# Kernel tuning notes

Measured on AMD Instinct MI355X. Metric: run time of the kernel, lower is better.

Reference implementation:

```python
import jax, jax.numpy as jnp
import numpy as np

N_NODES = 100000
N_EDGES = 3200000
N_FEAT = 128
N_GRAPHS = 64


def setup_inputs() -> dict:
    key = jax.random.key(0)
    ks = jax.random.split(key, 8)
    x = jax.random.normal(ks[0], (N_NODES, N_FEAT), dtype=jnp.float32)
    edge_index = jax.random.randint(ks[1], (2, N_EDGES), 0, N_NODES, dtype=jnp.int64)
    batch = jnp.sort(jax.random.randint(ks[2], (N_NODES,), 0, N_GRAPHS, dtype=jnp.int64))
    # GCNConv weights (glorot-style scale) and biases
    W1 = jax.random.normal(ks[3], (N_FEAT, 32), dtype=jnp.float32) / np.sqrt(N_FEAT)
    b1 = jnp.zeros((32,), dtype=jnp.float32)
    W2 = jax.random.normal(ks[4], (32, 16), dtype=jnp.float32) / np.sqrt(32.0)
    b2 = jnp.zeros((16,), dtype=jnp.float32)
    lin_w = jax.random.normal(ks[5], (16, 1), dtype=jnp.float32) / np.sqrt(16.0)
    lin_b = jnp.zeros((1,), dtype=jnp.float32)
    return {"x": x, "edge_index": edge_index, "batch": batch,
            "W1": W1, "b1": b1, "W2": W2, "b2": b2,
            "lin_w": lin_w, "lin_b": lin_b}


def _gcn_conv(x, W, b, src, dst, deg_inv_sqrt, n_nodes):
    # transform first (fewer features downstream when out_dim < in_dim)
    xw = x @ W  # [N, out]
    norm = deg_inv_sqrt[src] * deg_inv_sqrt[dst]  # [E+N]
    msg = xw[src] * norm[:, None]  # gather + scale
    out = jax.ops.segment_sum(msg, dst, num_segments=n_nodes)  # scatter-add
    return out + b


def reference(x, edge_index, batch, W1, b1, W2, b2, lin_w, lin_b):
    n_nodes = x.shape[0]
    self_loop = jnp.arange(n_nodes, dtype=edge_index.dtype)
    src = jnp.concatenate([edge_index[0], self_loop])
    dst = jnp.concatenate([edge_index[1], self_loop])
    # symmetric GCN normalization with self-loops
    deg = jax.ops.segment_sum(jnp.ones_like(src, dtype=x.dtype), dst,
                              num_segments=n_nodes)
    deg_inv_sqrt = jnp.where(deg > 0, jax.lax.rsqrt(jnp.maximum(deg, 1.0)), 0.0)

    h = _gcn_conv(x, W1, b1, src, dst, deg_inv_sqrt, n_nodes)
    h = jax.nn.relu(h)
    # F.dropout with training=False (eval) is identity
    h = _gcn_conv(h, W2, b2, src, dst, deg_inv_sqrt, n_nodes)

    # global_mean_pool over batch index
    sums = jax.ops.segment_sum(h, batch, num_segments=N_GRAPHS)  # [G,16]
    cnts = jax.ops.segment_sum(jnp.ones((n_nodes,), dtype=h.dtype), batch,
                               num_segments=N_GRAPHS)
    pooled = sums / jnp.maximum(cnts, 1.0)[:, None]
    return pooled @ lin_w + lin_b  # [G,1]
```

## Files before the change

kernel.cpp:

```cpp
#include <hip/hip_runtime.h>

#define NN 100000
#define NE 3200000
#define NF 128
#define C1 32
#define C2 16
#define NG 64
#define BKT_SH 7
#define BKT_W  128
#define NBKT   782
#define CH     8192
#define NW     391
#define RSTR   784
#define MAPCAP 6400

#define OFF_BCNT  0
#define OFF_POOL  1024
#define OFF_CNTF  2048
#define OFF_RUN   2304
#define OFF_ROW   308848
#define OFF_DIS   408864
#define OFF_EDG   508864
#define OFF_XS1   OFF_EDG
#define OFF_XS2B  (OFF_EDG + NE)
#define OFF_COL   (OFF_XS2B + NN*8)

__device__ __forceinline__ unsigned pack_bf2(float a, float b) {
    unsigned ua = __float_as_uint(a);
    unsigned ub = __float_as_uint(b);
    ua = (ua + 0x7fffu + ((ua >> 16) & 1u)) >> 16;
    ub = (ub + 0x7fffu + ((ub >> 16) & 1u)) & 0xffff0000u;
    return ua | ub;
}
__device__ __forceinline__ float2 unpack_bf2(unsigned u) {
    return make_float2(__uint_as_float(u << 16), __uint_as_float(u & 0xffff0000u));
}
__device__ __forceinline__ void accum8(float* a, uint4 q) {
    float2 f0 = unpack_bf2(q.x), f1 = unpack_bf2(q.y);
    float2 f2 = unpack_bf2(q.z), f3 = unpack_bf2(q.w);
    a[0] += f0.x; a[1] += f0.y; a[2] += f1.x; a[3] += f1.y;
    a[4] += f2.x; a[5] += f2.y; a[6] += f3.x; a[7] += f3.y;
}

__global__ __launch_bounds__(512) void k_part(
    const int* __restrict__ S, const int* __restrict__ D,
    unsigned* __restrict__ edgebuf, int* __restrict__ runstart,
    int* __restrict__ bcnt)
{
    __shared__ int lhist[1024];
    __shared__ int lstart[1024];
    __shared__ int lcur[NBKT];
    __shared__ int wsum[8];
    __shared__ unsigned lsort[CH];
    const int w = blockIdx.x;
    const int t = threadIdx.x;
    const int e0 = w * CH;
    const int n = min(CH, NE - e0);
    const int n4 = n >> 2;
    const int4* __restrict__ S4 = (const int4*)(S + e0);
    const int4* __restrict__ D4 = (const int4*)(D + e0);

    for (int i = t; i < 1024; i += 512) lhist[i] = 0;
    __syncthreads();
    for (int i = t; i < n4; i += 512) {
        int4 d = D4[i];
        atomicAdd(&lhist[(unsigned)d.x >> BKT_SH], 1);
        atomicAdd(&lhist[(unsigned)d.y >> BKT_SH], 1);
        atomicAdd(&lhist[(unsigned)d.z >> BKT_SH], 1);
        atomicAdd(&lhist[(unsigned)d.w >> BKT_SH], 1);
    }
    __syncthreads();
    for (int i = t; i < NBKT; i += 512) atomicAdd(&bcnt[i], lhist[i]);

    int c0 = lhist[t * 2 + 0], c1 = lhist[t * 2 + 1];
    int ts = c0 + c1;
    const int lane = t & 63, wv = t >> 6;
    int sc = ts;
    #pragma unroll
    for (int off = 1; off < 64; off <<= 1) {
        int v = __shfl_up(sc, off, 64);
        if (lane >= off) sc += v;
    }
    if (lane == 63) wsum[wv] = sc;
    __syncthreads();
    int wo = 0;
    #pragma unroll
    for (int i = 0; i < 8; ++i) wo += (i < wv) ? wsum[i] : 0;
    int excl = sc - ts + wo;
    lstart[t * 2 + 0] = excl;
    lstart[t * 2 + 1] = excl + c0;
    __syncthreads();

    for (int i = t; i < 783; i += 512) runstart[w * RSTR + i] = lstart[i];
    for (int i = t; i < NBKT; i += 512) lcur[i] = lstart[i];
    __syncthreads();
    for (int i = t; i < n4; i += 512) {
        int4 s = S4[i];
        int4 d = D4[i];
        { int p = atomicAdd(&lcur[(unsigned)d.x >> BKT_SH], 1);
          lsort[p] = ((unsigned)s.x << BKT_SH) | ((unsigned)d.x & (BKT_W - 1)); }
        { int p = atomicAdd(&lcur[(unsigned)d.y >> BKT_SH], 1);
          lsort[p] = ((unsigned)s.y << BKT_SH) | ((unsigned)d.y & (BKT_W - 1)); }
        { int p = atomicAdd(&lcur[(unsigned)d.z >> BKT_SH], 1);
          lsort[p] = ((unsigned)s.z << BKT_SH) | ((unsigned)d.z & (BKT_W - 1)); }
        { int p = atomicAdd(&lcur[(unsigned)d.w >> BKT_SH], 1);
          lsort[p] = ((unsigned)s.w << BKT_SH) | ((unsigned)d.w & (BKT_W - 1)); }
    }
    __syncthreads();
    {
        uint4* __restrict__ eb4 = (uint4*)(edgebuf + e0);
        const uint4* __restrict__ ls4 = (const uint4*)lsort;
        for (int i = t; i < n4; i += 512) eb4[i] = ls4[i];
    }
}

__global__ __launch_bounds__(256) void k_fillfused(
    const unsigned* __restrict__ edgebuf, const int* __restrict__ runstart,
    const int* __restrict__ bcnt,
    int* __restrict__ rowstart, float* __restrict__ dis, int* __restrict__ colidx)
{
    __shared__ int rl[NW];
    __shared__ int pfx[NW];
    __shared__ int basea[NW];
    __shared__ unsigned short map[MAPCAP];
    __shared__ int lcnt[BKT_W];
    __shared__ int lcur[BKT_W];
    __shared__ int wsum[4];
    __shared__ int hs1;
    const int b = blockIdx.x;
    const int t = threadIdx.x;
    const int lane = t & 63, wv = t >> 6;

    int accp = 0;
    for (int i = t; i < b; i += 256) accp += bcnt[i];
    #pragma unroll
    for (int off = 1; off < 64; off <<= 1) accp += __shfl_xor(accp, off, 64);
    if (lane == 0) wsum[wv] = accp;

    for (int w = t; w < NW; w += 256) {
        int s0 = runstart[w * RSTR + b];
        int s1 = runstart[w * RSTR + b + 1];
        basea[w] = s0;
        rl[w] = s1 - s0;
    }
    if (t < BKT_W) lcnt[t] = 0;
    __syncthreads();
    const int bs = wsum[0] + wsum[1] + wsum[2] + wsum[3];

    int w0 = t * 2;
    int c0 = (w0 < NW) ? rl[w0] : 0;
    int c1 = (w0 + 1 < NW) ? rl[w0 + 1] : 0;
    int ts = c0 + c1;
    int sc = ts;
    #pragma unroll
    for (int off = 1; off < 64; off <<= 1) {
        int v = __shfl_up(sc, off, 64);
        if (lane >= off) sc += v;
    }
    __syncthreads();
    if (lane == 63) wsum[wv] = sc;
    __syncthreads();
    int wo = 0;
    #pragma unroll
    for (int i = 0; i < 4; ++i) wo += (i < wv) ? wsum[i] : 0;
    const int total = wsum[0] + wsum[1] + wsum[2] + wsum[3];
    int excl0 = sc - ts + wo;
    if (w0 < NW)     pfx[w0]     = excl0;
    if (w0 + 1 < NW) pfx[w0 + 1] = excl0 + c0;
    __syncthreads();

    for (int w = t; w < NW; w += 256) {
        int p = pfx[w], len = rl[w];
        basea[w] = w * CH + basea[w] - p;
        for (int i = 0; i < len; ++i) map[p + i] = (unsigned short)w;
    }
    __syncthreads();
    for (int j = t; j < total; j += 256) {
        unsigned p = edgebuf[basea[map[j]] + j];
        atomicAdd(&lcnt[p & (BKT_W - 1)], 1);
    }
    __syncthreads();

    int myc = 0, sc2 = 0;
    if (t < BKT_W) {
        myc = lcnt[t];
        sc2 = myc;
        #pragma unroll
        for (int off = 1; off < 64; off <<= 1) {
            int v = __shfl_up(sc2, off, 64);
            if (lane >= off) sc2 += v;
        }
        if (t == 63) hs1 = sc2;
    }
    __syncthreads();
    if (t < BKT_W) {
        int excl = sc2 - myc + ((t >= 64) ? hs1 : 0);
        int node = b * BKT_W + t;
        if (node < NN) {
            rowstart[node] = bs + excl;
            dis[node] = rsqrtf((float)myc + 1.0f);
        }
        lcur[t] = bs + excl;
    }
    if (b == 0 && t == 0) rowstart[NN] = NE;
    __syncthreads();
    for (int j = t; j < total; j += 256) {
        unsigned p = edgebuf[basea[map[j]] + j];
        int pos = atomicAdd(&lcur[p & (BKT_W - 1)], 1);
        colidx[pos] = (int)(p >> BKT_SH);
    }
}

__global__ __launch_bounds__(256) void k_gemm1(
    const float* __restrict__ x, const float* __restrict__ W1,
    const float* __restrict__ dis,
    unsigned* __restrict__ xs1)
{
    __shared__ float xls[128 * 33];
    __shared__ float wls[32 * 32];
    const int t = threadIdx.x;
    const int tc = t & 7;
    const int tr = t >> 3;
    const int base = blockIdx.x * 128;

    float a[4][4] = {};

    for (int k0 = 0; k0 < NF; k0 += 32) {
        {
            int i = t * 4;
            int kk = i >> 5, c = i & 31;
            *(float4*)&wls[kk * 32 + c] = *(const float4*)&W1[(k0 + kk) * C1 + c];
        }
        #pragma unroll
        for (int r = 0; r < 4; ++r) {
            int n = (t >> 3) + r * 32;
            int j = (t & 7) * 4;
            int node = base + n;
            float4 v = make_float4(0.f, 0.f, 0.f, 0.f);
            if (node < NN) v = *(const float4*)&x[(long long)node * NF + k0 + j];
            xls[n * 33 + j + 0] = v.x;
            xls[n * 33 + j + 1] = v.y;
            xls[n * 33 + j + 2] = v.z;
            xls[n * 33 + j + 3] = v.w;
        }
        __syncthreads();
        #pragma unroll 8
        for (int kk = 0; kk < 32; ++kk) {
            float4 w = *(const float4*)&wls[kk * 32 + tc * 4];
            #pragma unroll
            for (int i = 0; i < 4; ++i) {
                float xv = xls[(tr * 4 + i) * 33 + kk];
                a[i][0] = fmaf(xv, w.x, a[i][0]);
                a[i][1] = fmaf(xv, w.y, a[i][1]);
                a[i][2] = fmaf(xv, w.z, a[i][2]);
                a[i][3] = fmaf(xv, w.w, a[i][3]);
            }
        }
        __syncthreads();
    }
    #pragma unroll
    for (int i = 0; i < 4; ++i) {
        int node = base + tr * 4 + i;
        if (node < NN) {
            float dv = dis[node];
            uint2 o;
            o.x = pack_bf2(a[i][0] * dv, a[i][1] * dv);
            o.y = pack_bf2(a[i][2] * dv, a[i][3] * dv);
            *(uint2*)&xs1[node * 16 + tc * 2] = o;
        }
    }
}

__global__ __launch_bounds__(256) void k_gather1(
    const unsigned* __restrict__ xs1, const int* __restrict__ colidx,
    const int* __restrict__ rowstart, const float* __restrict__ dis,
    const float* __restrict__ b1, const float* __restrict__ W2,
    unsigned* __restrict__ xs2b)
{
    __shared__ float w2s[C1 * C2];
    __shared__ float hrow[64 * 33];
    const int t = threadIdx.x;
    if (t < 128) *(float4*)&w2s[t * 4] = *(const float4*)&W2[t * 4];
    const int l = t & 3;
    const int n = t >> 2;
    const int v = blockIdx.x * 64 + n;
    const bool valid = v < NN;

    float a0[8] = {}, a1[8] = {};
    float dv = 0.f;
    if (valid) {
        const int start = rowstart[v];
        const int num = rowstart[v + 1] - start;
        const int* __restrict__ cp = &colidx[start];
        const uint4* __restrict__ tb = (const uint4*)xs1;
        accum8(a0, tb[v * 4 + l]);
        int i = 0;
        for (; i + 8 <= num; i += 8) {
            int s0 = cp[i],   s1 = cp[i+1], s2 = cp[i+2], s3 = cp[i+3];
            int s4 = cp[i+4], s5 = cp[i+5], s6 = cp[i+6], s7 = cp[i+7];
            uint4 q0 = tb[s0 * 4 + l];
            uint4 q1 = tb[s1 * 4 + l];
            uint4 q2 = tb[s2 * 4 + l];
            uint4 q3 = tb[s3 * 4 + l];
            uint4 q4 = tb[s4 * 4 + l];
            uint4 q5 = tb[s5 * 4 + l];
            uint4 q6 = tb[s6 * 4 + l];
            uint4 q7 = tb[s7 * 4 + l];
            accum8(a0, q0); accum8(a1, q1); accum8(a0, q2); accum8(a1, q3);
            accum8(a0, q4); accum8(a1, q5); accum8(a0, q6); accum8(a1, q7);
        }
        for (; i < num; ++i) accum8(a0, tb[cp[i] * 4 + l]);
        dv = dis[v];
        #pragma unroll
        for (int j = 0; j < 8; ++j) {
            float h = fmaxf(fmaf(a0[j] + a1[j], dv, b1[l * 8 + j]), 0.f);
            hrow[n * 33 + l * 8 + j] = h;
        }
    }
    __syncthreads();
    if (valid) {
        const float* hr = &hrow[n * 33];
        float s0 = 0.f, s1 = 0.f, s2 = 0.f, s3 = 0.f;
        #pragma unroll
        for (int k = 0; k < 32; ++k) {
            float hv = hr[k];
            s0 = fmaf(hv, w2s[k * C2 + l * 4 + 0], s0);
            s1 = fmaf(hv, w2s[k * C2 + l * 4 + 1], s1);
            s2 = fmaf(hv, w2s[k * C2 + l * 4 + 2], s2);
            s3 = fmaf(hv, w2s[k * C2 + l * 4 + 3], s3);
        }
        uint2 o;
        o.x = pack_bf2(s0 * dv, s1 * dv);
        o.y = pack_bf2(s2 * dv, s3 * dv);
        *(uint2*)&xs2b[v * 8 + l * 2] = o;
    }
}

__global__ __launch_bounds__(256) void k_gather2(
    const unsigned* __restrict__ xs2b, const int* __restrict__ colidx,
    const int* __restrict__ rowstart, const float* __restrict__ dis,
    const int* __restrict__ batch,
    float* __restrict__ pool, float* __restrict__ cntf)
{
    __shared__ float psum[NG * C2];
    __shared__ float cs[NG];
    const int t = threadIdx.x;
    for (int i = t; i < NG * C2; i += 256) psum[i] = 0.f;
    if (t < NG) cs[t] = 0.f;
    __syncthreads();

    const int l = t & 1;
    const int n = t >> 1;
    const int v = blockIdx.x * 128 + n;
    const bool valid = v < NN;
    const int lane = t & 63;

    float r[8] = {};
    int g = 0;
    if (valid) {
        const int start = rowstart[v];
        const int num = rowstart[v + 1] - start;
        const int* __restrict__ cp = &colidx[start];
        const uint4* __restrict__ tb = (const uint4*)xs2b;
        float a0[8] = {}, a1[8] = {};
        accum8(a0, tb[v * 2 + l]);
        int i = 0;
        for (; i + 8 <= num; i += 8) {
            int s0 = cp[i],   s1 = cp[i+1], s2 = cp[i+2], s3 = cp[i+3];
            int s4 = cp[i+4], s5 = cp[i+5], s6 = cp[i+6], s7 = cp[i+7];
            uint4 q0 = tb[s0 * 2 + l];
            uint4 q1 = tb[s1 * 2 + l];
            uint4 q2 = tb[s2 * 2 + l];
            uint4 q3 = tb[s3 * 2 + l];
            uint4 q4 = tb[s4 * 2 + l];
            uint4 q5 = tb[s5 * 2 + l];
            uint4 q6 = tb[s6 * 2 + l];
            uint4 q7 = tb[s7 * 2 + l];
            accum8(a0, q0); accum8(a1, q1); accum8(a0, q2); accum8(a1, q3);
            accum8(a0, q4); accum8(a1, q5); accum8(a0, q6); accum8(a1, q7);
        }
        for (; i < num; ++i) accum8(a0, tb[cp[i] * 2 + l]);
        float dv = dis[v];
        g = batch[v];
        #pragma unroll
        for (int j = 0; j < 8; ++j) r[j] = (a0[j] + a1[j]) * dv;
    }

    int g0 = __shfl(g, 0, 64);
    bool uni = __all(!valid || g == g0);
    if (uni) {
        #pragma unroll
        for (int j = 0; j < 8; ++j) {
            float val = r[j];
            val += __shfl_xor(val, 2, 64);
            val += __shfl_xor(val, 4, 64);
            val += __shfl_xor(val, 8, 64);
            val += __shfl_xor(val, 16, 64);
            val += __shfl_xor(val, 32, 64);
            if (lane < 2) atomicAdd(&psum[g0 * C2 + lane * 8 + j], val);
        }
        unsigned long long mb = __ballot(valid && (l == 0));
        if (lane == 0 && mb) atomicAdd(&cs[g0], (float)__popcll(mb));
    } else {
        if (valid) {
            #pragma unroll
            for (int j = 0; j < 8; ++j)
                atomicAdd(&psum[g * C2 + l * 8 + j], r[j]);
            if (l == 0) atomicAdd(&cs[g], 1.0f);
        }
    }
    __syncthreads();
    for (int i = t; i < NG * C2; i += 256)
        if (psum[i] != 0.f) atomicAdd(&pool[i], psum[i]);
    if (t < NG && cs[t] != 0.f) atomicAdd(&cntf[t], cs[t]);
}

__global__ void k_final(const float* __restrict__ pool, const float* __restrict__ cntf,
                        const float* __restrict__ b2,
                        const float* __restrict__ lw, const float* __restrict__ lb,
                        float* __restrict__ out)
{
    int g = threadIdx.x;
    if (g < NG) {
        float c = fmaxf(cntf[g], 1.0f);
        float inv = 1.0f / c;
        float s = lb[0];
        #pragma unroll
        for (int k = 0; k < C2; ++k) {
            s = fmaf(b2[k], lw[k], s);
            s = fmaf(pool[g * C2 + k] * inv, lw[k], s);
        }
        out[g] = s;
    }
}

extern "C" void kernel_launch(void* const* d_in, const int* in_sizes, int n_in,
                              void* d_out, int out_size, void* d_ws, size_t ws_size,
                              hipStream_t stream) {
    const float* x     = (const float*)d_in[0];
    const int*   ei    = (const int*)d_in[1];
    const int*   batch = (const int*)d_in[2];
    const float* W1    = (const float*)d_in[3];
    const float* b1    = (const float*)d_in[4];
    const float* W2    = (const float*)d_in[5];
    const float* b2    = (const float*)d_in[6];
    const float* lw    = (const float*)d_in[7];
    const float* lb    = (const float*)d_in[8];
    float* out = (float*)d_out;

    float*    wsf = (float*)d_ws;
    int*      wsi = (int*)d_ws;
    unsigned* wsu = (unsigned*)d_ws;

    int*      bcnt     = wsi + OFF_BCNT;
    float*    pool     = wsf + OFF_POOL;
    float*    cntf     = wsf + OFF_CNTF;
    int*      runstart = wsi + OFF_RUN;
    int*      rowstart = wsi + OFF_ROW;
    float*    dis      = wsf + OFF_DIS;
    unsigned* edgebuf  = wsu + OFF_EDG;
    unsigned* xs1      = wsu + OFF_XS1;
    unsigned* xs2b     = wsu + OFF_XS2B;
    int*      colidx   = wsi + OFF_COL;

    const int* S = ei;
    const int* D = ei + NE;

    hipMemsetAsync(wsi + OFF_BCNT, 0, 2304 * sizeof(int), stream);

    k_part       <<<NW, 512, 0, stream>>>(S, D, edgebuf, runstart, bcnt);
    k_fillfused  <<<NBKT, 256, 0, stream>>>(edgebuf, runstart, bcnt, rowstart, dis, colidx);
    k_gemm1      <<<(NN + 127) / 128, 256, 0, stream>>>(x, W1, dis, xs1);
    k_gather1    <<<(NN + 63) / 64, 256, 0, stream>>>(xs1, colidx, rowstart, dis, b1, W2, xs2b);
    k_gather2    <<<(NN + 127) / 128, 256, 0, stream>>>(xs2b, colidx, rowstart, dis, batch, pool, cntf);
    k_final      <<<1, 64, 0, stream>>>(pool, cntf, b2, lw, lb, out);
}
```

Measured before the change: 251.2 us.

## Split gather rows across more lanes and software-pipeline neighbor index loads

Both gather kernels now give each node twice as many threads, each loading an 8-byte bf16 slice instead of 16 bytes, and cut nodes per block to match. The inner loop prefetches the next eight column indices while the current eight feature loads are in flight, and uses four accumulators. The aim is more memory-level parallelism and more concurrent nodes in the latency-bound random gathers, at the cost of more threads and more index loads per edge. gather1 drops the bounds check because 100000 divides evenly by 32.

```diff
diff --git a/kernel.cpp b/kernel.cpp
--- a/kernel.cpp
+++ b/kernel.cpp
@@ -35,11 +35,9 @@
 __device__ __forceinline__ float2 unpack_bf2(unsigned u) {
     return make_float2(__uint_as_float(u << 16), __uint_as_float(u & 0xffff0000u));
 }
-__device__ __forceinline__ void accum8(float* a, uint4 q) {
+__device__ __forceinline__ void acc4(float4& a, uint2 q) {
     float2 f0 = unpack_bf2(q.x), f1 = unpack_bf2(q.y);
-    float2 f2 = unpack_bf2(q.z), f3 = unpack_bf2(q.w);
-    a[0] += f0.x; a[1] += f0.y; a[2] += f1.x; a[3] += f1.y;
-    a[4] += f2.x; a[5] += f2.y; a[6] += f3.x; a[7] += f3.y;
+    a.x += f0.x; a.y += f0.y; a.z += f1.x; a.w += f1.y;
 }
 
 __global__ __launch_bounds__(512) void k_part(
@@ -278,62 +276,68 @@
     unsigned* __restrict__ xs2b)
 {
     __shared__ float w2s[C1 * C2];
-    __shared__ float hrow[64 * 33];
+    __shared__ float hrow[32 * 33];
     const int t = threadIdx.x;
     if (t < 128) *(float4*)&w2s[t * 4] = *(const float4*)&W2[t * 4];
-    const int l = t & 3;
-    const int n = t >> 2;
-    const int v = blockIdx.x * 64 + n;
-    const bool valid = v < NN;
-
-    float a0[8] = {}, a1[8] = {};
-    float dv = 0.f;
-    if (valid) {
-        const int start = rowstart[v];
-        const int num = rowstart[v + 1] - start;
-        const int* __restrict__ cp = &colidx[start];
-        const uint4* __restrict__ tb = (const uint4*)xs1;
-        accum8(a0, tb[v * 4 + l]);
-        int i = 0;
-        for (; i + 8 <= num; i += 8) {
-            int s0 = cp[i],   s1 = cp[i+1], s2 = cp[i+2], s3 = cp[i+3];
-            int s4 = cp[i+4], s5 = cp[i+5], s6 = cp[i+6], s7 = cp[i+7];
-            uint4 q0 = tb[s0 * 4 + l];
-            uint4 q1 = tb[s1 * 4 + l];
-            uint4 q2 = tb[s2 * 4 + l];
-            uint4 q3 = tb[s3 * 4 + l];
-            uint4 q4 = tb[s4 * 4 + l];
-            uint4 q5 = tb[s5 * 4 + l];
-            uint4 q6 = tb[s6 * 4 + l];
-            uint4 q7 = tb[s7 * 4 + l];
-            accum8(a0, q0); accum8(a1, q1); accum8(a0, q2); accum8(a1, q3);
-            accum8(a0, q4); accum8(a1, q5); accum8(a0, q6); accum8(a1, q7);
-        }
-        for (; i < num; ++i) accum8(a0, tb[cp[i] * 4 + l]);
-        dv = dis[v];
+    const int l = t & 7;
+    const int n = t >> 3;
+    const int v = blockIdx.x * 32 + n;
+
+    const int start = rowstart[v];
+    const int num = rowstart[v + 1] - start;
+    const int* __restrict__ cp = &colidx[start];
+    const uint2* __restrict__ tb = (const uint2*)xs1;
+    float4 a0 = make_float4(0.f, 0.f, 0.f, 0.f);
+    float4 a1 = a0, a2 = a0, a3 = a0;
+    acc4(a0, tb[v * 8 + l]);
+    int i = 0;
+    if (num >= 8) {
+        int idx[8];
         #pragma unroll
-        for (int j = 0; j < 8; ++j) {
-            float h = fmaxf(fmaf(a0[j] + a1[j], dv, b1[l * 8 + j]), 0.f);
-            hrow[n * 33 + l * 8 + j] = h;
-        }
-    }
-    __syncthreads();
-    if (valid) {
-        const float* hr = &hrow[n * 33];
-        float s0 = 0.f, s1 = 0.f, s2 = 0.f, s3 = 0.f;
-        #pragma unroll
-        for (int k = 0; k < 32; ++k) {
-            float hv = hr[k];
-            s0 = fmaf(hv, w2s[k * C2 + l * 4 + 0], s0);
-            s1 = fmaf(hv, w2s[k * C2 + l * 4 + 1], s1);
-            s2 = fmaf(hv, w2s[k * C2 + l * 4 + 2], s2);
-            s3 = fmaf(hv, w2s[k * C2 + l * 4 + 3], s3);
-        }
-        uint2 o;
-        o.x = pack_bf2(s0 * dv, s1 * dv);
-        o.y = pack_bf2(s2 * dv, s3 * dv);
-        *(uint2*)&xs2b[v * 8 + l * 2] = o;
-    }
+        for (int j = 0; j < 8; ++j) idx[j] = cp[j];
+        for (; i + 16 <= num; i += 8) {
+            int nx[8];
+            #pragma unroll
+            for (int j = 0; j < 8; ++j) nx[j] = cp[i + 8 + j];
+            uint2 q[8];
+            #pragma unroll
+            for (int j = 0; j < 8; ++j) q[j] = tb[idx[j] * 8 + l];
+            acc4(a0, q[0]); acc4(a1, q[1]); acc4(a2, q[2]); acc4(a3, q[3]);
+            acc4(a0, q[4]); acc4(a1, q[5]); acc4(a2, q[6]); acc4(a3, q[7]);
+            #pragma unroll
+            for (int j = 0; j < 8; ++j) idx[j] = nx[j];
+        }
+        {
+            uint2 q[8];
+            #pragma unroll
+            for (int j = 0; j < 8; ++j) q[j] = tb[idx[j] * 8 + l];
+            acc4(a0, q[0]); acc4(a1, q[1]); acc4(a2, q[2]); acc4(a3, q[3]);
+            acc4(a0, q[4]); acc4(a1, q[5]); acc4(a2, q[6]); acc4(a3, q[7]);
+            i += 8;
+        }
+    }
+    for (; i < num; ++i) acc4(a0, tb[cp[i] * 8 + l]);
+    float ax = (a0.x + a1.x) + (a2.x + a3.x);
+    float ay = (a0.y + a1.y) + (a2.y + a3.y);
+    float az = (a0.z + a1.z) + (a2.z + a3.z);
+    float aw = (a0.w + a1.w) + (a2.w + a3.w);
+    const float dv = dis[v];
+
+    hrow[n * 33 + l * 4 + 0] = fmaxf(fmaf(ax, dv, b1[l * 4 + 0]), 0.f);
+    hrow[n * 33 + l * 4 + 1] = fmaxf(fmaf(ay, dv, b1[l * 4 + 1]), 0.f);
+    hrow[n * 33 + l * 4 + 2] = fmaxf(fmaf(az, dv, b1[l * 4 + 2]), 0.f);
+    hrow[n * 33 + l * 4 + 3] = fmaxf(fmaf(aw, dv, b1[l * 4 + 3]), 0.f);
+    __syncthreads();
+
+    const float* hr = &hrow[n * 33];
+    float s0 = 0.f, s1 = 0.f;
+    #pragma unroll
+    for (int k = 0; k < 32; ++k) {
+        float hv = hr[k];
+        s0 = fmaf(hv, w2s[k * C2 + 2 * l + 0], s0);
+        s1 = fmaf(hv, w2s[k * C2 + 2 * l + 1], s1);
+    }
+    xs2b[v * 8 + l] = pack_bf2(s0 * dv, s1 * dv);
 }
 
 __global__ __launch_bounds__(256) void k_gather2(
@@ -349,63 +353,78 @@
     if (t < NG) cs[t] = 0.f;
     __syncthreads();
 
-    const int l = t & 1;
-    const int n = t >> 1;
-    const int v = blockIdx.x * 128 + n;
+    const int l = t & 3;
+    const int n = t >> 2;
+    const int v = blockIdx.x * 64 + n;
     const bool valid = v < NN;
     const int lane = t & 63;
 
-    float r[8] = {};
+    float4 r = make_float4(0.f, 0.f, 0.f, 0.f);
     int g = 0;
     if (valid) {
         const int start = rowstart[v];
         const int num = rowstart[v + 1] - start;
         const int* __restrict__ cp = &colidx[start];
-        const uint4* __restrict__ tb = (const uint4*)xs2b;
-        float a0[8] = {}, a1[8] = {};
-        accum8(a0, tb[v * 2 + l]);
+        const uint2* __restrict__ tb = (const uint2*)xs2b;
+        float4 a0 = make_float4(0.f, 0.f, 0.f, 0.f);
+        float4 a1 = a0, a2 = a0, a3 = a0;
+        acc4(a0, tb[v * 4 + l]);
         int i = 0;
-        for (; i + 8 <= num; i += 8) {
-            int s0 = cp[i],   s1 = cp[i+1], s2 = cp[i+2], s3 = cp[i+3];
-            int s4 = cp[i+4], s5 = cp[i+5], s6 = cp[i+6], s7 = cp[i+7];
-            uint4 q0 = tb[s0 * 2 + l];
-            uint4 q1 = tb[s1 * 2 + l];
-            uint4 q2 = tb[s2 * 2 + l];
-            uint4 q3 = tb[s3 * 2 + l];
-            uint4 q4 = tb[s4 * 2 + l];
-            uint4 q5 = tb[s5 * 2 + l];
-            uint4 q6 = tb[s6 * 2 + l];
-            uint4 q7 = tb[s7 * 2 + l];
-            accum8(a0, q0); accum8(a1, q1); accum8(a0, q2); accum8(a1, q3);
-            accum8(a0, q4); accum8(a1, q5); accum8(a0, q6); accum8(a1, q7);
-        }
-        for (; i < num; ++i) accum8(a0, tb[cp[i] * 2 + l]);
+        if (num >= 8) {
+            int idx[8];
+            #pragma unroll
+            for (int j = 0; j < 8; ++j) idx[j] = cp[j];
+            for (; i + 16 <= num; i += 8) {
+                int nx[8];
+                #pragma unroll
+                for (int j = 0; j < 8; ++j) nx[j] = cp[i + 8 + j];
+                uint2 q[8];
+                #pragma unroll
+                for (int j = 0; j < 8; ++j) q[j] = tb[idx[j] * 4 + l];
+                acc4(a0, q[0]); acc4(a1, q[1]); acc4(a2, q[2]); acc4(a3, q[3]);
+                acc4(a0, q[4]); acc4(a1, q[5]); acc4(a2, q[6]); acc4(a3, q[7]);
+                #pragma unroll
+                for (int j = 0; j < 8; ++j) idx[j] = nx[j];
+            }
+            {
+                uint2 q[8];
+                #pragma unroll
+                for (int j = 0; j < 8; ++j) q[j] = tb[idx[j] * 4 + l];
+                acc4(a0, q[0]); acc4(a1, q[1]); acc4(a2, q[2]); acc4(a3, q[3]);
+                acc4(a0, q[4]); acc4(a1, q[5]); acc4(a2, q[6]); acc4(a3, q[7]);
+                i += 8;
+            }
+        }
+        for (; i < num; ++i) acc4(a0, tb[cp[i] * 4 + l]);
         float dv = dis[v];
         g = batch[v];
-        #pragma unroll
-        for (int j = 0; j < 8; ++j) r[j] = (a0[j] + a1[j]) * dv;
+        r.x = ((a0.x + a1.x) + (a2.x + a3.x)) * dv;
+        r.y = ((a0.y + a1.y) + (a2.y + a3.y)) * dv;
+        r.z = ((a0.z + a1.z) + (a2.z + a3.z)) * dv;
+        r.w = ((a0.w + a1.w) + (a2.w + a3.w)) * dv;
     }
 
     int g0 = __shfl(g, 0, 64);
     bool uni = __all(!valid || g == g0);
     if (uni) {
+        float vv[4] = {r.x, r.y, r.z, r.w};
         #pragma unroll
-        for (int j = 0; j < 8; ++j) {
-            float val = r[j];
-            val += __shfl_xor(val, 2, 64);
+        for (int j = 0; j < 4; ++j) {
+            float val = vv[j];
             val += __shfl_xor(val, 4, 64);
             val += __shfl_xor(val, 8, 64);
             val += __shfl_xor(val, 16, 64);
             val += __shfl_xor(val, 32, 64);
-            if (lane < 2) atomicAdd(&psum[g0 * C2 + lane * 8 + j], val);
+            if (lane < 4) atomicAdd(&psum[g0 * C2 + lane * 4 + j], val);
         }
         unsigned long long mb = __ballot(valid && (l == 0));
         if (lane == 0 && mb) atomicAdd(&cs[g0], (float)__popcll(mb));
     } else {
         if (valid) {
-            #pragma unroll
-            for (int j = 0; j < 8; ++j)
-                atomicAdd(&psum[g * C2 + l * 8 + j], r[j]);
+            atomicAdd(&psum[g * C2 + l * 4 + 0], r.x);
+            atomicAdd(&psum[g * C2 + l * 4 + 1], r.y);
+            atomicAdd(&psum[g * C2 + l * 4 + 2], r.z);
+            atomicAdd(&psum[g * C2 + l * 4 + 3], r.w);
             if (l == 0) atomicAdd(&cs[g], 1.0f);
         }
     }
@@ -471,7 +490,7 @@
     k_part       <<<NW, 512, 0, stream>>>(S, D, edgebuf, runstart, bcnt);
     k_fillfused  <<<NBKT, 256, 0, stream>>>(edgebuf, runstart, bcnt, rowstart, dis, colidx);
     k_gemm1      <<<(NN + 127) / 128, 256, 0, stream>>>(x, W1, dis, xs1);
-    k_gather1    <<<(NN + 63) / 64, 256, 0, stream>>>(xs1, colidx, rowstart, dis, b1, W2, xs2b);
-    k_gather2    <<<(NN + 127) / 128, 256, 0, stream>>>(xs2b, colidx, rowstart, dis, batch, pool, cntf);
+    k_gather1    <<<NN / 32, 256, 0, stream>>>(xs1, colidx, rowstart, dis, b1, W2, xs2b);
+    k_gather2    <<<(NN + 63) / 64, 256, 0, stream>>>(xs2b, colidx, rowstart, dis, batch, pool, cntf);
     k_final      <<<1, 64, 0, stream>>>(pool, cntf, b2, lw, lb, out);
 }
```

Measured after the change: 243.7 us. 3.0% less time.

## Split layer-1 gather into two feature halves with wavefront-per-node edge parallelism

Applied to the files above, without the earlier changes.

Layer-1 bf16 features are stored as two 16-column halves, and the layer-1 aggregation runs as two kernels, each gathering one half. Each kernel gives every node a full wavefront: 16 lanes stride over edges and 4 lanes over columns, then a shuffle tree reduces across edges. The goal is a smaller gather footprint per pass for better cache hit rates, and spreading long neighbour lists across more lanes. In exchange it adds a kernel launch, re-reads the CSR index twice, writes an fp32 intermediate to memory, and drops the warp-uniform pooling reduction in gather2 in favour of per-node shared atomics.

```diff
diff --git a/kernel.cpp b/kernel.cpp
--- a/kernel.cpp
+++ b/kernel.cpp
@@ -21,7 +21,9 @@
 #define OFF_ROW   308848
 #define OFF_DIS   408864
 #define OFF_EDG   508864
-#define OFF_XS1   OFF_EDG
+#define OFF_XS1H0 OFF_EDG
+#define OFF_XS1H1 (OFF_EDG + NN*8)
+#define OFF_H1A   (OFF_EDG + NN*16)
 #define OFF_XS2B  (OFF_EDG + NE)
 #define OFF_COL   (OFF_XS2B + NN*8)
 
@@ -35,11 +37,9 @@
 __device__ __forceinline__ float2 unpack_bf2(unsigned u) {
     return make_float2(__uint_as_float(u << 16), __uint_as_float(u & 0xffff0000u));
 }
-__device__ __forceinline__ void accum8(float* a, uint4 q) {
+__device__ __forceinline__ void acc4(float4& a, uint2 q) {
     float2 f0 = unpack_bf2(q.x), f1 = unpack_bf2(q.y);
-    float2 f2 = unpack_bf2(q.z), f3 = unpack_bf2(q.w);
-    a[0] += f0.x; a[1] += f0.y; a[2] += f1.x; a[3] += f1.y;
-    a[4] += f2.x; a[5] += f2.y; a[6] += f3.x; a[7] += f3.y;
+    a.x += f0.x; a.y += f0.y; a.z += f1.x; a.w += f1.y;
 }
 
 __global__ __launch_bounds__(512) void k_part(
@@ -214,7 +214,7 @@
 __global__ __launch_bounds__(256) void k_gemm1(
     const float* __restrict__ x, const float* __restrict__ W1,
     const float* __restrict__ dis,
-    unsigned* __restrict__ xs1)
+    unsigned* __restrict__ xs1h0, unsigned* __restrict__ xs1h1)
 {
     __shared__ float xls[128 * 33];
     __shared__ float wls[32 * 32];
@@ -266,73 +266,98 @@
             uint2 o;
             o.x = pack_bf2(a[i][0] * dv, a[i][1] * dv);
             o.y = pack_bf2(a[i][2] * dv, a[i][3] * dv);
-            *(uint2*)&xs1[node * 16 + tc * 2] = o;
-        }
-    }
-}
-
-__global__ __launch_bounds__(256) void k_gather1(
-    const unsigned* __restrict__ xs1, const int* __restrict__ colidx,
+            unsigned* dst = (tc < 4) ? &xs1h0[node * 8 + tc * 2]
+                                     : &xs1h1[node * 8 + (tc - 4) * 2];
+            *(uint2*)dst = o;
+        }
+    }
+}
+
+__device__ __forceinline__ float4 gather_half(
+    const uint2* __restrict__ tb, const int* __restrict__ cp,
+    int num, int v, int e, int l)
+{
+    float4 a = make_float4(0.f, 0.f, 0.f, 0.f);
+    if (e == 0) acc4(a, tb[v * 4 + l]);
+    int i = e;
+    for (; i + 16 < num; i += 32) {
+        int i0 = cp[i], i1 = cp[i + 16];
+        uint2 q0 = tb[i0 * 4 + l];
+        uint2 q1 = tb[i1 * 4 + l];
+        acc4(a, q0); acc4(a, q1);
+    }
+    if (i < num) acc4(a, tb[cp[i] * 4 + l]);
+    #pragma unroll
+    for (int m = 4; m < 64; m <<= 1) {
+        a.x += __shfl_xor(a.x, m, 64);
+        a.y += __shfl_xor(a.y, m, 64);
+        a.z += __shfl_xor(a.z, m, 64);
+        a.w += __shfl_xor(a.w, m, 64);
+    }
+    return a;
+}
+
+__global__ __launch_bounds__(256) void k_g1a(
+    const unsigned* __restrict__ xs1h0, const int* __restrict__ colidx,
     const int* __restrict__ rowstart, const float* __restrict__ dis,
-    const float* __restrict__ b1, const float* __restrict__ W2,
-    unsigned* __restrict__ xs2b)
+    const float* __restrict__ b1, float* __restrict__ h1a)
+{
+    const int t = threadIdx.x;
+    const int lane = t & 63;
+    const int v = blockIdx.x * 4 + (t >> 6);
+    const int l = lane & 3, e = lane >> 2;
+    const int start = rowstart[v];
+    const int num = rowstart[v + 1] - start;
+    float4 a = gather_half((const uint2*)xs1h0, &colidx[start], num, v, e, l);
+    if (e == 0) {
+        float dv = dis[v];
+        float4 o;
+        o.x = fmaxf(fmaf(a.x, dv, b1[l * 4 + 0]), 0.f);
+        o.y = fmaxf(fmaf(a.y, dv, b1[l * 4 + 1]), 0.f);
+        o.z = fmaxf(fmaf(a.z, dv, b1[l * 4 + 2]), 0.f);
+        o.w = fmaxf(fmaf(a.w, dv, b1[l * 4 + 3]), 0.f);
+        *(float4*)&h1a[v * 16 + l * 4] = o;
+    }
+}
+
+__global__ __launch_bounds__(256) void k_g1b(
+    const unsigned* __restrict__ xs1h1, const int* __restrict__ colidx,
+    const int* __restrict__ rowstart, const float* __restrict__ dis,
+    const float* __restrict__ b1, const float* __restrict__ h1a,
+    const float* __restrict__ W2, unsigned* __restrict__ xs2b)
 {
     __shared__ float w2s[C1 * C2];
-    __shared__ float hrow[64 * 33];
+    __shared__ float hrow[4][32];
     const int t = threadIdx.x;
     if (t < 128) *(float4*)&w2s[t * 4] = *(const float4*)&W2[t * 4];
-    const int l = t & 3;
-    const int n = t >> 2;
-    const int v = blockIdx.x * 64 + n;
-    const bool valid = v < NN;
-
-    float a0[8] = {}, a1[8] = {};
-    float dv = 0.f;
-    if (valid) {
-        const int start = rowstart[v];
-        const int num = rowstart[v + 1] - start;
-        const int* __restrict__ cp = &colidx[start];
-        const uint4* __restrict__ tb = (const uint4*)xs1;
-        accum8(a0, tb[v * 4 + l]);
-        int i = 0;
-        for (; i + 8 <= num; i += 8) {
-            int s0 = cp[i],   s1 = cp[i+1], s2 = cp[i+2], s3 = cp[i+3];
-            int s4 = cp[i+4], s5 = cp[i+5], s6 = cp[i+6], s7 = cp[i+7];
-            uint4 q0 = tb[s0 * 4 + l];
-            uint4 q1 = tb[s1 * 4 + l];
-            uint4 q2 = tb[s2 * 4 + l];
-            uint4 q3 = tb[s3 * 4 + l];
-            uint4 q4 = tb[s4 * 4 + l];
-            uint4 q5 = tb[s5 * 4 + l];
-            uint4 q6 = tb[s6 * 4 + l];
-            uint4 q7 = tb[s7 * 4 + l];
-            accum8(a0, q0); accum8(a1, q1); accum8(a0, q2); accum8(a1, q3);
-            accum8(a0, q4); accum8(a1, q5); accum8(a0, q6); accum8(a1, q7);
-        }
-        for (; i < num; ++i) accum8(a0, tb[cp[i] * 4 + l]);
-        dv = dis[v];
-        #pragma unroll
-        for (int j = 0; j < 8; ++j) {
-            float h = fmaxf(fmaf(a0[j] + a1[j], dv, b1[l * 8 + j]), 0.f);
-            hrow[n * 33 + l * 8 + j] = h;
-        }
-    }
-    __syncthreads();
-    if (valid) {
-        const float* hr = &hrow[n * 33];
-        float s0 = 0.f, s1 = 0.f, s2 = 0.f, s3 = 0.f;
+    const int lane = t & 63, wv = t >> 6;
+    const int v = blockIdx.x * 4 + wv;
+    const int l = lane & 3, e = lane >> 2;
+    const int start = rowstart[v];
+    const int num = rowstart[v + 1] - start;
+    float4 a = gather_half((const uint2*)xs1h1, &colidx[start], num, v, e, l);
+    const float dv = dis[v];
+    if (e == 0) {
+        float4 hl = *(const float4*)&h1a[v * 16 + l * 4];
+        *(float4*)&hrow[wv][l * 4] = hl;
+        float4 o;
+        o.x = fmaxf(fmaf(a.x, dv, b1[16 + l * 4 + 0]), 0.f);
+        o.y = fmaxf(fmaf(a.y, dv, b1[16 + l * 4 + 1]), 0.f);
+        o.z = fmaxf(fmaf(a.z, dv, b1[16 + l * 4 + 2]), 0.f);
+        o.w = fmaxf(fmaf(a.w, dv, b1[16 + l * 4 + 3]), 0.f);
+        *(float4*)&hrow[wv][16 + l * 4] = o;
+    }
+    __syncthreads();
+    if (lane < 8) {
+        const float* hr = hrow[wv];
+        float s0 = 0.f, s1 = 0.f;
         #pragma unroll
         for (int k = 0; k < 32; ++k) {
             float hv = hr[k];
-            s0 = fmaf(hv, w2s[k * C2 + l * 4 + 0], s0);
-            s1 = fmaf(hv, w2s[k * C2 + l * 4 + 1], s1);
-            s2 = fmaf(hv, w2s[k * C2 + l * 4 + 2], s2);
-            s3 = fmaf(hv, w2s[k * C2 + l * 4 + 3], s3);
-        }
-        uint2 o;
-        o.x = pack_bf2(s0 * dv, s1 * dv);
-        o.y = pack_bf2(s2 * dv, s3 * dv);
-        *(uint2*)&xs2b[v * 8 + l * 2] = o;
+            s0 = fmaf(hv, w2s[k * C2 + 2 * lane + 0], s0);
+            s1 = fmaf(hv, w2s[k * C2 + 2 * lane + 1], s1);
+        }
+        xs2b[v * 8 + lane] = pack_bf2(s0 * dv, s1 * dv);
     }
 }
 
@@ -349,65 +374,20 @@
     if (t < NG) cs[t] = 0.f;
     __syncthreads();
 
-    const int l = t & 1;
-    const int n = t >> 1;
-    const int v = blockIdx.x * 128 + n;
-    const bool valid = v < NN;
     const int lane = t & 63;
-
-    float r[8] = {};
-    int g = 0;
-    if (valid) {
-        const int start = rowstart[v];
-        const int num = rowstart[v + 1] - start;
-        const int* __restrict__ cp = &colidx[start];
-        const uint4* __restrict__ tb = (const uint4*)xs2b;
-        float a0[8] = {}, a1[8] = {};
-        accum8(a0, tb[v * 2 + l]);
-        int i = 0;
-        for (; i + 8 <= num; i += 8) {
-            int s0 = cp[i],   s1 = cp[i+1], s2 = cp[i+2], s3 = cp[i+3];
-            int s4 = cp[i+4], s5 = cp[i+5], s6 = cp[i+6], s7 = cp[i+7];
-            uint4 q0 = tb[s0 * 2 + l];
-            uint4 q1 = tb[s1 * 2 + l];
-            uint4 q2 = tb[s2 * 2 + l];
-            uint4 q3 = tb[s3 * 2 + l];
-            uint4 q4 = tb[s4 * 2 + l];
-            uint4 q5 = tb[s5 * 2 + l];
-            uint4 q6 = tb[s6 * 2 + l];
-            uint4 q7 = tb[s7 * 2 + l];
-            accum8(a0, q0); accum8(a1, q1); accum8(a0, q2); accum8(a1, q3);
-            accum8(a0, q4); accum8(a1, q5); accum8(a0, q6); accum8(a1, q7);
-        }
-        for (; i < num; ++i) accum8(a0, tb[cp[i] * 2 + l]);
+    const int v = blockIdx.x * 4 + (t >> 6);
+    const int l = lane & 3, e = lane >> 2;
+    const int start = rowstart[v];
+    const int num = rowstart[v + 1] - start;
+    float4 a = gather_half((const uint2*)xs2b, &colidx[start], num, v, e, l);
+    if (e == 0) {
         float dv = dis[v];
-        g = batch[v];
-        #pragma unroll
-        for (int j = 0; j < 8; ++j) r[j] = (a0[j] + a1[j]) * dv;
-    }
-
-    int g0 = __shfl(g, 0, 64);
-    bool uni = __all(!valid || g == g0);
-    if (uni) {
-        #pragma unroll
-        for (int j = 0; j < 8; ++j) {
-            float val = r[j];
-            val += __shfl_xor(val, 2, 64);
-            val += __shfl_xor(val, 4, 64);
-            val += __shfl_xor(val, 8, 64);
-            val += __shfl_xor(val, 16, 64);
-            val += __shfl_xor(val, 32, 64);
-            if (lane < 2) atomicAdd(&psum[g0 * C2 + lane * 8 + j], val);
-        }
-        unsigned long long mb = __ballot(valid && (l == 0));
-        if (lane == 0 && mb) atomicAdd(&cs[g0], (float)__popcll(mb));
-    } else {
-        if (valid) {
-            #pragma unroll
-            for (int j = 0; j < 8; ++j)
-                atomicAdd(&psum[g * C2 + l * 8 + j], r[j]);
-            if (l == 0) atomicAdd(&cs[g], 1.0f);
-        }
+        int g = batch[v];
+        atomicAdd(&psum[g * C2 + l * 4 + 0], a.x * dv);
+        atomicAdd(&psum[g * C2 + l * 4 + 1], a.y * dv);
+        atomicAdd(&psum[g * C2 + l * 4 + 2], a.z * dv);
+        atomicAdd(&psum[g * C2 + l * 4 + 3], a.w * dv);
+        if (l == 0) atomicAdd(&cs[g], 1.0f);
     }
     __syncthreads();
     for (int i = t; i < NG * C2; i += 256)
@@ -459,7 +439,9 @@
     int*      rowstart = wsi + OFF_ROW;
     float*    dis      = wsf + OFF_DIS;
     unsigned* edgebuf  = wsu + OFF_EDG;
-    unsigned* xs1      = wsu + OFF_XS1;
+    unsigned* xs1h0    = wsu + OFF_XS1H0;
+    unsigned* xs1h1    = wsu + OFF_XS1H1;
+    float*    h1a      = wsf + OFF_H1A;
     unsigned* xs2b     = wsu + OFF_XS2B;
     int*      colidx   = wsi + OFF_COL;
 
@@ -470,8 +452,9 @@
 
     k_part       <<<NW, 512, 0, stream>>>(S, D, edgebuf, runstart, bcnt);
     k_fillfused  <<<NBKT, 256, 0, stream>>>(edgebuf, runstart, bcnt, rowstart, dis, colidx);
-    k_gemm1      <<<(NN + 127) / 128, 256, 0, stream>>>(x, W1, dis, xs1);
-    k_gather1    <<<(NN + 63) / 64, 256, 0, stream>>>(xs1, colidx, rowstart, dis, b1, W2, xs2b);
-    k_gather2    <<<(NN + 127) / 128, 256, 0, stream>>>(xs2b, colidx, rowstart, dis, batch, pool, cntf);
+    k_gemm1      <<<(NN + 127) / 128, 256, 0, stream>>>(x, W1, dis, xs1h0, xs1h1);
+    k_g1a        <<<NN / 4, 256, 0, stream>>>(xs1h0, colidx, rowstart, dis, b1, h1a);
+    k_g1b        <<<NN / 4, 256, 0, stream>>>(xs1h1, colidx, rowstart, dis, b1, h1a, W2, xs2b);
+    k_gather2    <<<NN / 4, 256, 0, stream>>>(xs2b, colidx, rowstart, dis, batch, pool, cntf);
     k_final      <<<1, 64, 0, stream>>>(pool, cntf, b2, lw, lb, out);
 }
```

After: 497.1 us. +97.9%, slower.
